# Kernel tuning notes

Measured on AMD Instinct MI355X. Metric: run time of the kernel, lower is better.

Reference implementation:

```python
import jax, jax.numpy as jnp
import numpy as np

SCALE = 2
K = 8


def setup_inputs() -> dict:
    key = jax.random.key(0)
    k1, k2, k3 = jax.random.split(key, 3)
    m, f = 8192, 512
    y_patch = jax.random.normal(k1, (m, 64), dtype=jnp.float32)
    yd_patch = jax.random.normal(k2, (m, f), dtype=jnp.float32)
    idx_k = jax.random.randint(k3, (1, m, K), 0, m, dtype=jnp.int64)
    return {"y_patch": y_patch, "yd_patch": yd_patch, "idx_k": idx_k}


def reference(y_patch, yd_patch, idx_k):
    # y_patch: (m, f_q) -- only its leading dim m is used
    # yd_patch: (m, f) database features; idx_k: (1, m, k) neighbor indices into m
    m = y_patch.shape[0]
    yd = yd_patch.reshape(m, -1)          # (m=n, f)
    f = yd.shape[1]
    k = idx_k.shape[2]
    # Gather: torch builds z of shape (1, m, f, k) with z[0,q,c,j] = yd[idx_k[0,q,j], c].
    # Equivalent direct gather without materializing the expanded (1,m,f,n) tensor:
    z = yd[idx_k[0]]                      # (m, k, f)
    # torch permute(0,3,2,1): (1, m, f, k) -> (1, k, f, m)
    z = jnp.transpose(z, (1, 2, 0))       # (k, f, m)
    # view(1, k, f//scale, scale, m) then view(1, k*(f//scale), m*scale):
    # contiguous row-major, so a single reshape is exact.
    z_sr = z.reshape(1, k * (f // SCALE), m * SCALE)
    return z_sr
```

## Files before the change

kernel.cpp:

```cpp
#include <hip/hip_runtime.h>


#define QT 128
#define CT 32
#define QPAD 132
#define THREADS 256

typedef float f32x4 __attribute__((ext_vector_type(4)));

__global__ __launch_bounds__(THREADS, 4) void gather_transpose_kernel(
    const float* __restrict__ yd, const int* __restrict__ idx,
    float* __restrict__ out, int m, int f, int k)
{
    const int cb = blockIdx.x * CT;
    const int qb = blockIdx.y * QT;
    const int j  = blockIdx.z;
    const int t  = threadIdx.x;

    __shared__ int rows[QT];
    __shared__ float lds[CT][QPAD];

    if (t < QT) rows[t] = idx[(size_t)(qb + t) * k + j];
    __syncthreads();

    #pragma unroll
    for (int it = 0; it < (QT * CT / 4) / THREADS; ++it) {
        const int gid = it * THREADS + t;
        const int row = gid >> 3;
        const int ch  = gid & 7;
        const f32x4 v = *reinterpret_cast<const f32x4*>(
            yd + (size_t)rows[row] * f + cb + (ch << 2));
        const int c0 = ch << 2;
        lds[c0 + 0][row] = v.x;
        lds[c0 + 1][row] = v.y;
        lds[c0 + 2][row] = v.z;
        lds[c0 + 3][row] = v.w;
    }
    __syncthreads();

    const size_t outb = (size_t)j * f * m + (size_t)cb * m + qb;
    #pragma unroll
    for (int it = 0; it < (QT * CT / 4) / THREADS; ++it) {
        const int gid = it * THREADS + t;
        const int c  = gid >> 5;
        const int q4 = gid & 31;
        const f32x4 v = *reinterpret_cast<const f32x4*>(&lds[c][q4 << 2]);
        __builtin_nontemporal_store(v, reinterpret_cast<f32x4*>(
            out + outb + (size_t)c * m + (q4 << 2)));
    }
}

extern "C" void kernel_launch(void* const* d_in, const int* in_sizes, int n_in,
                              void* d_out, int out_size, void* d_ws, size_t ws_size,
                              hipStream_t stream) {
    const float* yd = (const float*)d_in[1];
    const int* idx = (const int*)d_in[2];
    float* out = (float*)d_out;

    const int m = in_sizes[0] / 64;
    const int f = in_sizes[1] / m;
    const int k = in_sizes[2] / m;

    dim3 grid(f / CT, m / QT, k);
    hipLaunchKernelGGL(gather_transpose_kernel, grid, dim3(THREADS), 0,
                       stream, yd, idx, out, m, f, k);
}
```

Before: 163.1 us.

## Process multiple tiles per block with register-prefetched gathers overlapping stores

```diff
diff --git a/kernel.cpp b/kernel.cpp
--- a/kernel.cpp
+++ b/kernel.cpp
@@ -5,48 +5,77 @@
 #define CT 32
 #define QPAD 132
 #define THREADS 256
+#define TPB 4
 
 typedef float f32x4 __attribute__((ext_vector_type(4)));
 
 __global__ __launch_bounds__(THREADS, 4) void gather_transpose_kernel(
     const float* __restrict__ yd, const int* __restrict__ idx,
-    float* __restrict__ out, int m, int f, int k)
+    float* __restrict__ out, int m, int f, int k, int tiles_per_j)
 {
-    const int cb = blockIdx.x * CT;
-    const int qb = blockIdx.y * QT;
-    const int j  = blockIdx.z;
+    __shared__ float lds[CT][QPAD];
     const int t  = threadIdx.x;
+    const int ch = t & 7;
+    const int r0 = t >> 3;
+    const int gridP = gridDim.x;
 
-    __shared__ int rows[QT];
-    __shared__ float lds[CT][QPAD];
+    int tile = blockIdx.x;
+    int j  = tile / tiles_per_j;
+    int r  = tile - j * tiles_per_j;
+    int cb = (r & 15) * CT;
+    int qb = (r >> 4) * QT;
 
-    if (t < QT) rows[t] = idx[(size_t)(qb + t) * k + j];
-    __syncthreads();
+    f32x4 d[4];
+    #pragma unroll
+    for (int l = 0; l < 4; ++l) {
+        const int row = r0 + (l << 5);
+        const int rr = idx[(size_t)(qb + row) * k + j];
+        d[l] = *reinterpret_cast<const f32x4*>(
+            yd + (size_t)rr * f + cb + (ch << 2));
+    }
 
     #pragma unroll
-    for (int it = 0; it < (QT * CT / 4) / THREADS; ++it) {
-        const int gid = it * THREADS + t;
-        const int row = gid >> 3;
-        const int ch  = gid & 7;
-        const f32x4 v = *reinterpret_cast<const f32x4*>(
-            yd + (size_t)rows[row] * f + cb + (ch << 2));
-        const int c0 = ch << 2;
-        lds[c0 + 0][row] = v.x;
-        lds[c0 + 1][row] = v.y;
-        lds[c0 + 2][row] = v.z;
-        lds[c0 + 3][row] = v.w;
-    }
-    __syncthreads();
+    for (int it = 0; it < TPB; ++it) {
+        __syncthreads();
+        {
+            const int c0 = ch << 2;
+            #pragma unroll
+            for (int l = 0; l < 4; ++l) {
+                const int row = r0 + (l << 5);
+                lds[c0 + 0][row] = d[l].x;
+                lds[c0 + 1][row] = d[l].y;
+                lds[c0 + 2][row] = d[l].z;
+                lds[c0 + 3][row] = d[l].w;
+            }
+        }
+        const int cur_cb = cb, cur_qb = qb, cur_j = j;
 
-    const size_t outb = (size_t)j * f * m + (size_t)cb * m + qb;
-    #pragma unroll
-    for (int it = 0; it < (QT * CT / 4) / THREADS; ++it) {
-        const int gid = it * THREADS + t;
-        const int c  = gid >> 5;
-        const int q4 = gid & 31;
-        const f32x4 v = *reinterpret_cast<const f32x4*>(&lds[c][q4 << 2]);
-        __builtin_nontemporal_store(v, reinterpret_cast<f32x4*>(
-            out + outb + (size_t)c * m + (q4 << 2)));
+        if (it + 1 < TPB) {
+            tile += gridP;
+            j  = tile / tiles_per_j;
+            r  = tile - j * tiles_per_j;
+            cb = (r & 15) * CT;
+            qb = (r >> 4) * QT;
+            #pragma unroll
+            for (int l = 0; l < 4; ++l) {
+                const int row = r0 + (l << 5);
+                const int rr = idx[(size_t)(qb + row) * k + j];
+                d[l] = *reinterpret_cast<const f32x4*>(
+                    yd + (size_t)rr * f + cb + (ch << 2));
+            }
+        }
+
+        __syncthreads();
+        const size_t outb = (size_t)cur_j * f * m + (size_t)cur_cb * m + cur_qb;
+        #pragma unroll
+        for (int l = 0; l < 4; ++l) {
+            const int gid = l * THREADS + t;
+            const int c  = gid >> 5;
+            const int q4 = gid & 31;
+            const f32x4 v = *reinterpret_cast<const f32x4*>(&lds[c][q4 << 2]);
+            __builtin_nontemporal_store(v, reinterpret_cast<f32x4*>(
+                out + outb + (size_t)c * m + (q4 << 2)));
+        }
     }
 }
 
@@ -61,7 +90,9 @@
     const int f = in_sizes[1] / m;
     const int k = in_sizes[2] / m;
 
-    dim3 grid(f / CT, m / QT, k);
+    const int tiles_per_j = (m / QT) * (f / CT);
+    const int ntiles = tiles_per_j * k;
+    dim3 grid(ntiles / TPB);
     hipLaunchKernelGGL(gather_transpose_kernel, grid, dim3(THREADS), 0,
-                       stream, yd, idx, out, m, f, k);
+                       stream, yd, idx, out, m, f, k, tiles_per_j);
 }
```

Result: no change. 164.5 us (+0.8%).
